# Kernel optimization log

Measured on AMD Instinct MI355X. Metric: run time of the kernel, lower is better.

The kernel has to match this reference:

```python
import jax, jax.numpy as jnp
import numpy as np

B, T, C, E, TOPK = 4, 4096, 1024, 8, 2
H = 4 * C

def setup_inputs() -> dict:
    key = jax.random.key(0)
    ks = jax.random.split(key, 8)
    s = 1.0 / np.sqrt(C)
    sh = 1.0 / np.sqrt(H)
    return {
        "x": jax.random.normal(ks[0], (B, T, C), jnp.float32),
        "noise_eps": jax.random.normal(ks[1], (B, T, E), jnp.float32),
        "route_w": jax.random.normal(ks[2], (C, E), jnp.float32) * s,
        "route_b": jnp.zeros((E,), jnp.float32),
        "noise_w": jax.random.normal(ks[3], (C, E), jnp.float32) * s,
        "noise_b": jnp.zeros((E,), jnp.float32),
        "w1": jax.random.normal(ks[4], (E, C, H), jnp.float32) * s,
        "b1": jnp.zeros((E, H), jnp.float32),
        "w2": jax.random.normal(ks[5], (E, H, C), jnp.float32) * sh,
        "b2": jnp.zeros((E, C), jnp.float32),
        "top_k": TOPK,
    }

def reference(x, noise_eps, route_w, route_b, noise_w, noise_b, w1, b1, w2, b2, top_k):
    Bq, Tq, Cq = x.shape
    nE = route_w.shape[1]
    xf = x.reshape(Bq * Tq, Cq)                      # [N, C]
    N = xf.shape[0]
    logits = xf @ route_w + route_b                   # [N, E]
    std = jax.nn.softplus(xf @ noise_w + noise_b)     # [N, E]
    noisy = logits + noise_eps.reshape(N, nE) * std   # [N, E]
    _, top_idx = jax.lax.top_k(noisy, top_k)          # [N, K]
    rows = jnp.arange(N)[:, None]
    mask = jnp.zeros((N, nE), bool).at[rows, top_idx].set(True)
    # softmax over only the selected logits (others -> prob 0)
    probs = jax.nn.softmax(jnp.where(mask, noisy, -jnp.inf), axis=-1)  # [N, E]
    out = jnp.zeros_like(xf)
    for e in range(nE):  # small fixed expert count
        h = jax.nn.relu(xf @ w1[e] + b1[e])           # [N, 4C]
        y = h @ w2[e] + b2[e]                         # [N, C]
        out = out + probs[:, e:e + 1] * y             # prob==0 for unrouted tokens
    return out.reshape(Bq, Tq, Cq)
```

## Files before the change

kernel.cpp:

```cpp
#include <hip/hip_runtime.h>
#include <hip/hip_bf16.h>
#include <stdint.h>

#define NC 1024
#define NE 8
#define NH 4096
#define NN 16384

typedef __bf16 bf16x8_t __attribute__((ext_vector_type(8)));
typedef float f32x4_t __attribute__((ext_vector_type(4)));

__device__ __forceinline__ void cvt8(const float4 a, const float4 b, __bf16* dst) {
  bf16x8_t r;
  r[0] = (__bf16)a.x; r[1] = (__bf16)a.y; r[2] = (__bf16)a.z; r[3] = (__bf16)a.w;
  r[4] = (__bf16)b.x; r[5] = (__bf16)b.y; r[6] = (__bf16)b.z; r[7] = (__bf16)b.w;
  *(bf16x8_t*)dst = r;
}

__global__ __launch_bounds__(256) void routing_kernel(
    const float* __restrict__ x, const float* __restrict__ eps,
    const float* __restrict__ rw, const float* __restrict__ rb,
    const float* __restrict__ nw, const float* __restrict__ nb,
    int* __restrict__ eidx, float2* __restrict__ pp2) {
  const int lane = threadIdx.x & 63;
  const int n = blockIdx.x * 4 + (threadIdx.x >> 6);
  if (n >= NN) return;
  double acc[16];
#pragma unroll
  for (int i = 0; i < 16; ++i) acc[i] = 0.0;
  const float* xr = x + (size_t)n * NC;
  for (int c0 = 0; c0 < NC; c0 += 64) {
    const int c = c0 + lane;
    const float xv = xr[c];
    const float4 r0 = *(const float4*)(rw + (size_t)c * NE);
    const float4 r1 = *(const float4*)(rw + (size_t)c * NE + 4);
    const float4 n0 = *(const float4*)(nw + (size_t)c * NE);
    const float4 n1 = *(const float4*)(nw + (size_t)c * NE + 4);
    acc[0] += (double)xv * r0.x;  acc[1] += (double)xv * r0.y;
    acc[2] += (double)xv * r0.z;  acc[3] += (double)xv * r0.w;
    acc[4] += (double)xv * r1.x;  acc[5] += (double)xv * r1.y;
    acc[6] += (double)xv * r1.z;  acc[7] += (double)xv * r1.w;
    acc[8] += (double)xv * n0.x;  acc[9] += (double)xv * n0.y;
    acc[10] += (double)xv * n0.z; acc[11] += (double)xv * n0.w;
    acc[12] += (double)xv * n1.x; acc[13] += (double)xv * n1.y;
    acc[14] += (double)xv * n1.z; acc[15] += (double)xv * n1.w;
  }
#pragma unroll
  for (int off = 32; off > 0; off >>= 1) {
#pragma unroll
    for (int i = 0; i < 16; ++i) acc[i] += __shfl_xor(acc[i], off, 64);
  }
  if (lane == 0) {
    double noisy[NE];
#pragma unroll
    for (int e = 0; e < NE; ++e) {
      const double lg = acc[e] + (double)rb[e];
      const double z = acc[8 + e] + (double)nb[e];
      const double sp = log1p(exp(-fabs(z))) + fmax(z, 0.0);
      noisy[e] = lg + (double)eps[(size_t)n * NE + e] * sp;
    }
    int i1 = -1, i2 = -1;
    double v1 = -1e300, v2 = -1e300;
#pragma unroll
    for (int e = 0; e < NE; ++e) {
      const double v = noisy[e];
      if (v > v1) { v2 = v1; i2 = i1; v1 = v; i1 = e; }
      else if (v > v2) { v2 = v; i2 = e; }
    }
    if (i1 < 0) i1 = 0;
    if (i2 < 0 || i2 == i1) i2 = (i1 + 1) & 7;
    const double d = exp(v2 - v1);
    const float p1 = (float)(1.0 / (1.0 + d));
    const float p2 = (float)(d / (1.0 + d));
    eidx[n] = i1 | (i2 << 8);
    pp2[n] = float2{p1, p2};
  }
}

__global__ __launch_bounds__(256) void build_lists(
    const int* __restrict__ eidx, const float2* __restrict__ pp2,
    int* __restrict__ counts, int* __restrict__ perm, float* __restrict__ pprob) {
  __shared__ int hist[NE];
  __shared__ int base[NE];
  const int t = threadIdx.x;
  if (t < NE) hist[t] = 0;
  __syncthreads();
  const int n = blockIdx.x * 256 + t;
  const int packed = eidx[n];
  const int e1 = packed & 255;
  const int e2 = (packed >> 8) & 255;
  const float2 p = pp2[n];
  const int l1 = atomicAdd(&hist[e1], 1);
  const int l2 = atomicAdd(&hist[e2], 1);
  __syncthreads();
  if (t < NE) base[t] = atomicAdd(&counts[t], hist[t]);
  __syncthreads();
  const int o1 = base[e1] + l1;
  const int o2 = base[e2] + l2;
  perm[e1 * NN + o1] = n; pprob[e1 * NN + o1] = p.x;
  perm[e2 * NN + o2] = n; pprob[e2 * NN + o2] = p.y;
}

__global__ __launch_bounds__(256) void transpose_cvt(
    const float* __restrict__ src, __bf16* __restrict__ dst, int R, int Cc) {
  __shared__ __align__(16) __bf16 tile[64][72];
  const int r0 = blockIdx.y * 64, c0 = blockIdx.x * 64;
  const int t = threadIdx.x;
  const int tr = t >> 3;
  const int tc = (t & 7) * 8;
#pragma unroll
  for (int h = 0; h < 2; ++h) {
    const int r = tr + h * 32;
    const float* sp = src + (size_t)(r0 + r) * Cc + (c0 + tc);
    const float4 a = *(const float4*)sp;
    const float4 b = *(const float4*)(sp + 4);
    cvt8(a, b, &tile[r][tc]);
  }
  __syncthreads();
#pragma unroll
  for (int h = 0; h < 2; ++h) {
    const int c = tr + h * 32;
    __bf16 tmp[8] __attribute__((aligned(16)));
#pragma unroll
    for (int j = 0; j < 8; ++j) tmp[j] = tile[tc + j][c];
    __bf16* dp = dst + (size_t)(c0 + c) * R + (r0 + tc);
    *(uint4*)dp = *(const uint4*)tmp;
  }
}

template<bool FASTB>
__global__ __launch_bounds__(256) void moe_gemm1(
    const float* __restrict__ x, const void* __restrict__ bsrc,
    const float* __restrict__ bias, __bf16* __restrict__ hbuf,
    const int* __restrict__ counts_e, const int* __restrict__ perm_e, int chunk_start) {
  int cnt = *counts_e; if (cnt > NN) cnt = NN; if (cnt < 0) cnt = 0;
  const int lr0 = blockIdx.y * 128;
  const int row0 = chunk_start + lr0;
  if (row0 >= cnt) return;
  const int t = threadIdx.x;

  __shared__ __align__(16) __bf16 As[128 * 32];
  __shared__ __align__(16) __bf16 Bs[128 * 32];

  const int ar1 = row0 + (t >> 2), ar2 = ar1 + 64;
  const int tokA = (ar1 < cnt) ? perm_e[ar1] : 0;
  const int tokB = (ar2 < cnt) ? perm_e[ar2] : 0;
  const int kg = (t & 3) * 8;
  const float* pA1 = x + (size_t)tokA * NC + kg;
  const float* pA2 = x + (size_t)tokB * NC + kg;
  const int n0 = blockIdx.x * 128;

  const __bf16* pB1 = nullptr; const __bf16* pB2 = nullptr;
  const float* pBw = nullptr;
  const int kk = t >> 3, cc = (t & 7) * 16;
  if (FASTB) {
    const __bf16* bt = (const __bf16*)bsrc;
    const int nrow = n0 + (t >> 2);
    pB1 = bt + (size_t)nrow * NC + kg;
    pB2 = bt + (size_t)(nrow + 64) * NC + kg;
  } else {
    pBw = (const float*)bsrc + (size_t)kk * NH + n0 + cc;
  }

  f32x4_t acc[4][4];
#pragma unroll
  for (int i = 0; i < 4; ++i)
#pragma unroll
    for (int j = 0; j < 4; ++j)
#pragma unroll
      for (int k = 0; k < 4; ++k) acc[i][j][k] = 0.f;

  const int lane = t & 63, wid = t >> 6;
  const int wm = (wid >> 1) * 64, wn = (wid & 1) * 64;
  const int col16 = lane & 15, quad = lane >> 4;
  const int a_off = (wm + col16) * 32 + quad * 8;
  const int b_off = (wn + col16) * 32 + quad * 8;

  for (int k0 = 0; k0 < NC; k0 += 32) {
    const float4 a1a = *(const float4*)(pA1 + k0);
    const float4 a1b = *(const float4*)(pA1 + k0 + 4);
    const float4 a2a = *(const float4*)(pA2 + k0);
    const float4 a2b = *(const float4*)(pA2 + k0 + 4);
    uint4 vb1, vb2; float4 w0, w1, w2, w3;
    if (FASTB) {
      vb1 = *(const uint4*)(pB1 + k0);
      vb2 = *(const uint4*)(pB2 + k0);
    } else {
      const float* pw = pBw + (size_t)k0 * NH;
      w0 = *(const float4*)pw; w1 = *(const float4*)(pw + 4);
      w2 = *(const float4*)(pw + 8); w3 = *(const float4*)(pw + 12);
    }
    __syncthreads();
    cvt8(a1a, a1b, As + t * 8);
    cvt8(a2a, a2b, As + 2048 + t * 8);
    if (FASTB) {
      *(uint4*)(Bs + t * 8) = vb1;
      *(uint4*)(Bs + 2048 + t * 8) = vb2;
    } else {
      cvt8(w0, w1, Bs + kk * 128 + cc);
      cvt8(w2, w3, Bs + kk * 128 + cc + 8);
    }
    __syncthreads();
    bf16x8_t af[4], bfr[4];
#pragma unroll
    for (int mi = 0; mi < 4; ++mi) af[mi] = *(const bf16x8_t*)(As + a_off + mi * 512);
    if (FASTB) {
#pragma unroll
      for (int ni = 0; ni < 4; ++ni) bfr[ni] = *(const bf16x8_t*)(Bs + b_off + ni * 512);
    } else {
#pragma unroll
      for (int ni = 0; ni < 4; ++ni) {
        const int bn = wn + ni * 16 + col16;
#pragma unroll
        for (int j = 0; j < 8; ++j) bfr[ni][j] = Bs[(quad * 8 + j) * 128 + bn];
      }
    }
#pragma unroll
    for (int mi = 0; mi < 4; ++mi)
#pragma unroll
      for (int ni = 0; ni < 4; ++ni)
        acc[mi][ni] = __builtin_amdgcn_mfma_f32_16x16x32_bf16(af[mi], bfr[ni], acc[mi][ni], 0, 0, 0);
  }

  const int colbase = n0 + wn + col16;
#pragma unroll
  for (int mi = 0; mi < 4; ++mi)
#pragma unroll
    for (int reg = 0; reg < 4; ++reg) {
      const int lr = lr0 + wm + mi * 16 + quad * 4 + reg;
      if (chunk_start + lr < cnt) {
        __bf16* hp = hbuf + (size_t)lr * NH + colbase;
#pragma unroll
        for (int ni = 0; ni < 4; ++ni) {
          const float v = acc[mi][ni][reg] + bias[colbase + ni * 16];
          hp[ni * 16] = (__bf16)fmaxf(v, 0.f);
        }
      }
    }
}

template<bool FASTB>
__global__ __launch_bounds__(256) void moe_gemm2(
    const __bf16* __restrict__ hbuf, const void* __restrict__ bsrc,
    const float* __restrict__ bias, float* __restrict__ out,
    const int* __restrict__ counts_e, const int* __restrict__ perm_e,
    const float* __restrict__ pprob_e, int chunk_start) {
  int cnt = *counts_e; if (cnt > NN) cnt = NN; if (cnt < 0) cnt = 0;
  const int lr0 = blockIdx.y * 128;
  if (chunk_start + lr0 >= cnt) return;
  const int t = threadIdx.x;

  __shared__ __align__(16) __bf16 As[128 * 32];
  __shared__ __align__(16) __bf16 Bs[128 * 32];

  const int lar1 = lr0 + (t >> 2);
  const int kg = (t & 3) * 8;
  const __bf16* pA1 = hbuf + (size_t)lar1 * NH + kg;
  const __bf16* pA2 = pA1 + (size_t)64 * NH;
  const int n0 = blockIdx.x * 128;

  const __bf16* pB1 = nullptr; const __bf16* pB2 = nullptr;
  const float* pBw = nullptr;
  const int kk = t >> 3, cc = (t & 7) * 16;
  if (FASTB) {
    const __bf16* bt = (const __bf16*)bsrc;
    const int nrow = n0 + (t >> 2);
    pB1 = bt + (size_t)nrow * NH + kg;
    pB2 = bt + (size_t)(nrow + 64) * NH + kg;
  } else {
    pBw = (const float*)bsrc + (size_t)kk * NC + n0 + cc;
  }

  f32x4_t acc[4][4];
#pragma unroll
  for (int i = 0; i < 4; ++i)
#pragma unroll
    for (int j = 0; j < 4; ++j)
#pragma unroll
      for (int k = 0; k < 4; ++k) acc[i][j][k] = 0.f;

  const int lane = t & 63, wid = t >> 6;
  const int wm = (wid >> 1) * 64, wn = (wid & 1) * 64;
  const int col16 = lane & 15, quad = lane >> 4;
  const int a_off = (wm + col16) * 32 + quad * 8;
  const int b_off = (wn + col16) * 32 + quad * 8;

  for (int k0 = 0; k0 < NH; k0 += 32) {
    const uint4 va1 = *(const uint4*)(pA1 + k0);
    const uint4 va2 = *(const uint4*)(pA2 + k0);
    uint4 vb1, vb2; float4 w0, w1, w2, w3;
    if (FASTB) {
      vb1 = *(const uint4*)(pB1 + k0);
      vb2 = *(const uint4*)(pB2 + k0);
    } else {
      const float* pw = pBw + (size_t)k0 * NC;
      w0 = *(const float4*)pw; w1 = *(const float4*)(pw + 4);
      w2 = *(const float4*)(pw + 8); w3 = *(const float4*)(pw + 12);
    }
    __syncthreads();
    *(uint4*)(As + t * 8) = va1;
    *(uint4*)(As + 2048 + t * 8) = va2;
    if (FASTB) {
      *(uint4*)(Bs + t * 8) = vb1;
      *(uint4*)(Bs + 2048 + t * 8) = vb2;
    } else {
      cvt8(w0, w1, Bs + kk * 128 + cc);
      cvt8(w2, w3, Bs + kk * 128 + cc + 8);
    }
    __syncthreads();
    bf16x8_t af[4], bfr[4];
#pragma unroll
    for (int mi = 0; mi < 4; ++mi) af[mi] = *(const bf16x8_t*)(As + a_off + mi * 512);
    if (FASTB) {
#pragma unroll
      for (int ni = 0; ni < 4; ++ni) bfr[ni] = *(const bf16x8_t*)(Bs + b_off + ni * 512);
    } else {
#pragma unroll
      for (int ni = 0; ni < 4; ++ni) {
        const int bn = wn + ni * 16 + col16;
#pragma unroll
        for (int j = 0; j < 8; ++j) bfr[ni][j] = Bs[(quad * 8 + j) * 128 + bn];
      }
    }
#pragma unroll
    for (int mi = 0; mi < 4; ++mi)
#pragma unroll
      for (int ni = 0; ni < 4; ++ni)
        acc[mi][ni] = __builtin_amdgcn_mfma_f32_16x16x32_bf16(af[mi], bfr[ni], acc[mi][ni], 0, 0, 0);
  }

  const int colbase = n0 + wn + col16;
#pragma unroll
  for (int mi = 0; mi < 4; ++mi)
#pragma unroll
    for (int reg = 0; reg < 4; ++reg) {
      const int lr = lr0 + wm + mi * 16 + quad * 4 + reg;
      const int r = chunk_start + lr;
      if (r < cnt) {
        const int tok = perm_e[r];
        const float p = pprob_e[r];
        float* op = out + (size_t)tok * NC + colbase;
#pragma unroll
        for (int ni = 0; ni < 4; ++ni) {
          op[ni * 16] += (acc[mi][ni][reg] + bias[colbase + ni * 16]) * p;
        }
      }
    }
}

extern "C" void kernel_launch(void* const* d_in, const int* in_sizes, int n_in,
                              void* d_out, int out_size, void* d_ws, size_t ws_size,
                              hipStream_t stream) {
  (void)in_sizes; (void)n_in;
  const float* x   = (const float*)d_in[0];
  const float* eps = (const float*)d_in[1];
  const float* rw  = (const float*)d_in[2];
  const float* rb  = (const float*)d_in[3];
  const float* nw  = (const float*)d_in[4];
  const float* nb  = (const float*)d_in[5];
  const float* w1  = (const float*)d_in[6];
  const float* b1  = (const float*)d_in[7];
  const float* w2  = (const float*)d_in[8];
  const float* b2  = (const float*)d_in[9];
  float* out = (float*)d_out;

  char* wsb = (char*)d_ws;
  int* counts = (int*)wsb;
  int* perm = (int*)(wsb + 256);
  float* pprob = (float*)(wsb + 256 + (size_t)NE * NN * 4);
  int* eidx = (int*)(wsb + 256 + (size_t)NE * NN * 8);
  float2* pp2 = (float2*)(wsb + 256 + (size_t)NE * NN * 8 + (size_t)NN * 4);
  size_t off = 256 + (size_t)NE * NN * 8 + (size_t)NN * 12;

  const size_t wtile = (size_t)NC * NH * 2;
  const bool fast = ws_size >= off + 2 * wtile + (size_t)128 * NH * 2 + (1u << 20);
  __bf16* w1t = nullptr; __bf16* w2t = nullptr;
  if (fast) {
    w1t = (__bf16*)(wsb + off); off += wtile;
    w2t = (__bf16*)(wsb + off); off += wtile;
  }
  __bf16* hbuf = (__bf16*)(wsb + off);
  const size_t remain = (ws_size > off) ? (ws_size - off) : 0;
  long rows_cap = (long)(remain / ((size_t)NH * 2));
  rows_cap = (rows_cap / 128) * 128;
  if (rows_cap > NN) rows_cap = NN;
  if (rows_cap < 128) rows_cap = 128;

  hipMemsetAsync(counts, 0, 256, stream);
  hipMemsetAsync(d_out, 0, (size_t)out_size * 4, stream);

  routing_kernel<<<NN / 4, 256, 0, stream>>>(x, eps, rw, rb, nw, nb, eidx, pp2);
  build_lists<<<NN / 256, 256, 0, stream>>>(eidx, pp2, counts, perm, pprob);

  const int nchunks = (int)((NN + rows_cap - 1) / rows_cap);
  for (int e = 0; e < NE; ++e) {
    const float* w1e = w1 + (size_t)e * NC * NH;
    const float* w2e = w2 + (size_t)e * NH * NC;
    if (fast) {
      transpose_cvt<<<dim3(NH / 64, NC / 64), 256, 0, stream>>>(w1e, w1t, NC, NH);
      transpose_cvt<<<dim3(NC / 64, NH / 64), 256, 0, stream>>>(w2e, w2t, NH, NC);
    }
    for (int ch = 0; ch < nchunks; ++ch) {
      const int cs = ch * (int)rows_cap;
      if (fast) {
        moe_gemm1<true><<<dim3(NH / 128, (unsigned)(rows_cap / 128)), 256, 0, stream>>>(
            x, w1t, b1 + (size_t)e * NH, hbuf, counts + e, perm + (size_t)e * NN, cs);
        moe_gemm2<true><<<dim3(NC / 128, (unsigned)(rows_cap / 128)), 256, 0, stream>>>(
            hbuf, w2t, b2 + (size_t)e * NC, out, counts + e, perm + (size_t)e * NN,
            pprob + (size_t)e * NN, cs);
      } else {
        moe_gemm1<false><<<dim3(NH / 128, (unsigned)(rows_cap / 128)), 256, 0, stream>>>(
            x, w1e, b1 + (size_t)e * NH, hbuf, counts + e, perm + (size_t)e * NN, cs);
        moe_gemm2<false><<<dim3(NC / 128, (unsigned)(rows_cap / 128)), 256, 0, stream>>>(
            hbuf, w2e, b2 + (size_t)e * NC, out, counts + e, perm + (size_t)e * NN,
            pprob + (size_t)e * NN, cs);
      }
    }
  }
}
```

Measured before the change: 1.892 ms.

## Split-K the second expert GEMM across four wave groups with shared-memory reduction

The down-projection GEMM now launches 1024-thread blocks in which four 256-thread groups each process one quarter of the K=4096 dimension, then sum their partial accumulators through shared memory before the first group writes the output. The aim is more parallelism and memory-level concurrency for gemm2, whose grid (8 column tiles by the row tiles) is small. The cost is 64KB of LDS per block, extra reduction syncs, and 1024-thread blocks that force tighter register limits (possible spills with 64 accumulator floats per thread).

Result: no change. 1.868 ms (-1.3%).

```diff
diff --git a/kernel.cpp b/kernel.cpp
--- a/kernel.cpp
+++ b/kernel.cpp
@@ -240,7 +240,7 @@
 }
 
 template<bool FASTB>
-__global__ __launch_bounds__(256) void moe_gemm2(
+__global__ __launch_bounds__(1024) void moe_gemm2(
     const __bf16* __restrict__ hbuf, const void* __restrict__ bsrc,
     const float* __restrict__ bias, float* __restrict__ out,
     const int* __restrict__ counts_e, const int* __restrict__ perm_e,
@@ -249,26 +249,30 @@
   const int lr0 = blockIdx.y * 128;
   if (chunk_start + lr0 >= cnt) return;
   const int t = threadIdx.x;
-
-  __shared__ __align__(16) __bf16 As[128 * 32];
-  __shared__ __align__(16) __bf16 Bs[128 * 32];
-
-  const int lar1 = lr0 + (t >> 2);
-  const int kg = (t & 3) * 8;
-  const __bf16* pA1 = hbuf + (size_t)lar1 * NH + kg;
+  const int ksub = t >> 8;
+  const int tt = t & 255;
+
+  __shared__ __align__(16) __bf16 smem[32768];
+  __bf16* As = smem + ksub * 4096;
+  __bf16* Bs = smem + 16384 + ksub * 4096;
+
+  const int lar1 = lr0 + (tt >> 2);
+  const int kg = (tt & 3) * 8;
+  const int kbase = ksub * (NH / 4);
+  const __bf16* pA1 = hbuf + (size_t)lar1 * NH + kbase + kg;
   const __bf16* pA2 = pA1 + (size_t)64 * NH;
   const int n0 = blockIdx.x * 128;
 
   const __bf16* pB1 = nullptr; const __bf16* pB2 = nullptr;
   const float* pBw = nullptr;
-  const int kk = t >> 3, cc = (t & 7) * 16;
+  const int kk = tt >> 3, cc = (tt & 7) * 16;
   if (FASTB) {
     const __bf16* bt = (const __bf16*)bsrc;
-    const int nrow = n0 + (t >> 2);
-    pB1 = bt + (size_t)nrow * NH + kg;
-    pB2 = bt + (size_t)(nrow + 64) * NH + kg;
+    const int nrow = n0 + (tt >> 2);
+    pB1 = bt + (size_t)nrow * NH + kbase + kg;
+    pB2 = bt + (size_t)(nrow + 64) * NH + kbase + kg;
   } else {
-    pBw = (const float*)bsrc + (size_t)kk * NC + n0 + cc;
+    pBw = (const float*)bsrc + (size_t)(kbase + kk) * NC + n0 + cc;
   }
 
   f32x4_t acc[4][4];
@@ -279,13 +283,13 @@
 #pragma unroll
       for (int k = 0; k < 4; ++k) acc[i][j][k] = 0.f;
 
-  const int lane = t & 63, wid = t >> 6;
+  const int lane = tt & 63, wid = tt >> 6;
   const int wm = (wid >> 1) * 64, wn = (wid & 1) * 64;
   const int col16 = lane & 15, quad = lane >> 4;
   const int a_off = (wm + col16) * 32 + quad * 8;
   const int b_off = (wn + col16) * 32 + quad * 8;
 
-  for (int k0 = 0; k0 < NH; k0 += 32) {
+  for (int k0 = 0; k0 < NH / 4; k0 += 32) {
     const uint4 va1 = *(const uint4*)(pA1 + k0);
     const uint4 va2 = *(const uint4*)(pA2 + k0);
     uint4 vb1, vb2; float4 w0, w1, w2, w3;
@@ -298,11 +302,11 @@
       w2 = *(const float4*)(pw + 8); w3 = *(const float4*)(pw + 12);
     }
     __syncthreads();
-    *(uint4*)(As + t * 8) = va1;
-    *(uint4*)(As + 2048 + t * 8) = va2;
-    if (FASTB) {
-      *(uint4*)(Bs + t * 8) = vb1;
-      *(uint4*)(Bs + 2048 + t * 8) = vb2;
+    *(uint4*)(As + tt * 8) = va1;
+    *(uint4*)(As + 2048 + tt * 8) = va2;
+    if (FASTB) {
+      *(uint4*)(Bs + tt * 8) = vb1;
+      *(uint4*)(Bs + 2048 + tt * 8) = vb2;
     } else {
       cvt8(w0, w1, Bs + kk * 128 + cc);
       cvt8(w2, w3, Bs + kk * 128 + cc + 8);
@@ -328,6 +332,28 @@
       for (int ni = 0; ni < 4; ++ni)
         acc[mi][ni] = __builtin_amdgcn_mfma_f32_16x16x32_bf16(af[mi], bfr[ni], acc[mi][ni], 0, 0, 0);
   }
+
+  __syncthreads();
+  f32x4_t* red = (f32x4_t*)smem;
+  for (int r = 1; r < 4; ++r) {
+    if (ksub == r) {
+#pragma unroll
+      for (int mi = 0; mi < 4; ++mi)
+#pragma unroll
+        for (int ni = 0; ni < 4; ++ni)
+          red[(mi * 4 + ni) * 256 + tt] = acc[mi][ni];
+    }
+    __syncthreads();
+    if (ksub == 0) {
+#pragma unroll
+      for (int mi = 0; mi < 4; ++mi)
+#pragma unroll
+        for (int ni = 0; ni < 4; ++ni)
+          acc[mi][ni] += red[(mi * 4 + ni) * 256 + tt];
+    }
+    __syncthreads();
+  }
+  if (ksub != 0) return;
 
   const int colbase = n0 + wn + col16;
 #pragma unroll
@@ -405,13 +431,13 @@
       if (fast) {
         moe_gemm1<true><<<dim3(NH / 128, (unsigned)(rows_cap / 128)), 256, 0, stream>>>(
             x, w1t, b1 + (size_t)e * NH, hbuf, counts + e, perm + (size_t)e * NN, cs);
-        moe_gemm2<true><<<dim3(NC / 128, (unsigned)(rows_cap / 128)), 256, 0, stream>>>(
+        moe_gemm2<true><<<dim3(NC / 128, (unsigned)(rows_cap / 128)), 1024, 0, stream>>>(
             hbuf, w2t, b2 + (size_t)e * NC, out, counts + e, perm + (size_t)e * NN,
             pprob + (size_t)e * NN, cs);
       } else {
         moe_gemm1<false><<<dim3(NH / 128, (unsigned)(rows_cap / 128)), 256, 0, stream>>>(
             x, w1e, b1 + (size_t)e * NH, hbuf, counts + e, perm + (size_t)e * NN, cs);
-        moe_gemm2<false><<<dim3(NC / 128, (unsigned)(rows_cap / 128)), 256, 0, stream>>>(
+        moe_gemm2<false><<<dim3(NC / 128, (unsigned)(rows_cap / 128)), 1024, 0, stream>>>(
             hbuf, w2e, b2 + (size_t)e * NC, out, counts + e, perm + (size_t)e * NN,
             pprob + (size_t)e * NN, cs);
       }
```

## Double-buffer LDS tiles with register prefetch and XOR swizzle in MoE GEMMs

Applied to the files above, without the earlier changes.

In the FASTB path of both expert GEMM kernels, the shared-memory A/B tiles are now double-buffered and the next k-slice is prefetched into registers while MFMAs run, so each iteration needs one barrier instead of two. The LDS layout also gets an XOR swizzle on the 8-element column groups to cut bank conflicts on fragment reads. The cost is twice the shared memory per block, which may lower occupancy, plus more registers held live for the prefetch.

Result: faster. 1.717 ms (-9.2%).

```diff
diff --git a/kernel.cpp b/kernel.cpp
--- a/kernel.cpp
+++ b/kernel.cpp
@@ -128,6 +128,7 @@
   }
 }
 
+
 template<bool FASTB>
 __global__ __launch_bounds__(256) void moe_gemm1(
     const float* __restrict__ x, const void* __restrict__ bsrc,
@@ -139,8 +140,8 @@
   if (row0 >= cnt) return;
   const int t = threadIdx.x;
 
-  __shared__ __align__(16) __bf16 As[128 * 32];
-  __shared__ __align__(16) __bf16 Bs[128 * 32];
+  __shared__ __align__(16) __bf16 As[2 * 128 * 32];
+  __shared__ __align__(16) __bf16 Bs[2 * 128 * 32];
 
   const int ar1 = row0 + (t >> 2), ar2 = ar1 + 64;
   const int tokA = (ar1 < cnt) ? perm_e[ar1] : 0;
@@ -173,53 +174,81 @@
   const int lane = t & 63, wid = t >> 6;
   const int wm = (wid >> 1) * 64, wn = (wid & 1) * 64;
   const int col16 = lane & 15, quad = lane >> 4;
-  const int a_off = (wm + col16) * 32 + quad * 8;
-  const int b_off = (wn + col16) * 32 + quad * 8;
-
-  for (int k0 = 0; k0 < NC; k0 += 32) {
-    const float4 a1a = *(const float4*)(pA1 + k0);
-    const float4 a1b = *(const float4*)(pA1 + k0 + 4);
-    const float4 a2a = *(const float4*)(pA2 + k0);
-    const float4 a2b = *(const float4*)(pA2 + k0 + 4);
-    uint4 vb1, vb2; float4 w0, w1, w2, w3;
-    if (FASTB) {
-      vb1 = *(const uint4*)(pB1 + k0);
-      vb2 = *(const uint4*)(pB2 + k0);
-    } else {
+
+  if (FASTB) {
+    const int woff = (t >> 2) * 32 + (((t & 3) ^ ((t >> 3) & 3)) * 8);
+    const int sel = (col16 >> 1) & 3;
+    const int a_off = (wm + col16) * 32 + ((quad ^ sel) * 8);
+    const int b_off = (wn + col16) * 32 + ((quad ^ sel) * 8);
+
+    float4 a1a = *(const float4*)(pA1);
+    float4 a1b = *(const float4*)(pA1 + 4);
+    float4 a2a = *(const float4*)(pA2);
+    float4 a2b = *(const float4*)(pA2 + 4);
+    uint4 vb1 = *(const uint4*)(pB1);
+    uint4 vb2 = *(const uint4*)(pB2);
+    int cur = 0;
+    for (int k0 = 0; k0 < NC; k0 += 32) {
+      __bf16* Asc = As + cur * 4096;
+      __bf16* Bsc = Bs + cur * 4096;
+      cvt8(a1a, a1b, Asc + woff);
+      cvt8(a2a, a2b, Asc + 2048 + woff);
+      *(uint4*)(Bsc + woff) = vb1;
+      *(uint4*)(Bsc + 2048 + woff) = vb2;
+      if (k0 + 32 < NC) {
+        a1a = *(const float4*)(pA1 + k0 + 32);
+        a1b = *(const float4*)(pA1 + k0 + 36);
+        a2a = *(const float4*)(pA2 + k0 + 32);
+        a2b = *(const float4*)(pA2 + k0 + 36);
+        vb1 = *(const uint4*)(pB1 + k0 + 32);
+        vb2 = *(const uint4*)(pB2 + k0 + 32);
+      }
+      __syncthreads();
+      bf16x8_t af[4], bfr[4];
+#pragma unroll
+      for (int mi = 0; mi < 4; ++mi) af[mi] = *(const bf16x8_t*)(Asc + a_off + mi * 512);
+#pragma unroll
+      for (int ni = 0; ni < 4; ++ni) bfr[ni] = *(const bf16x8_t*)(Bsc + b_off + ni * 512);
+#pragma unroll
+      for (int mi = 0; mi < 4; ++mi)
+#pragma unroll
+        for (int ni = 0; ni < 4; ++ni)
+          acc[mi][ni] = __builtin_amdgcn_mfma_f32_16x16x32_bf16(af[mi], bfr[ni], acc[mi][ni], 0, 0, 0);
+      cur ^= 1;
+    }
+  } else {
+    const int a_off = (wm + col16) * 32 + quad * 8;
+    for (int k0 = 0; k0 < NC; k0 += 32) {
+      const float4 a1a = *(const float4*)(pA1 + k0);
+      const float4 a1b = *(const float4*)(pA1 + k0 + 4);
+      const float4 a2a = *(const float4*)(pA2 + k0);
+      const float4 a2b = *(const float4*)(pA2 + k0 + 4);
       const float* pw = pBw + (size_t)k0 * NH;
-      w0 = *(const float4*)pw; w1 = *(const float4*)(pw + 4);
-      w2 = *(const float4*)(pw + 8); w3 = *(const float4*)(pw + 12);
-    }
-    __syncthreads();
-    cvt8(a1a, a1b, As + t * 8);
-    cvt8(a2a, a2b, As + 2048 + t * 8);
-    if (FASTB) {
-      *(uint4*)(Bs + t * 8) = vb1;
-      *(uint4*)(Bs + 2048 + t * 8) = vb2;
-    } else {
+      const float4 w0 = *(const float4*)pw;
+      const float4 w1 = *(const float4*)(pw + 4);
+      const float4 w2 = *(const float4*)(pw + 8);
+      const float4 w3 = *(const float4*)(pw + 12);
+      __syncthreads();
+      cvt8(a1a, a1b, As + t * 8);
+      cvt8(a2a, a2b, As + 2048 + t * 8);
       cvt8(w0, w1, Bs + kk * 128 + cc);
       cvt8(w2, w3, Bs + kk * 128 + cc + 8);
-    }
-    __syncthreads();
-    bf16x8_t af[4], bfr[4];
-#pragma unroll
-    for (int mi = 0; mi < 4; ++mi) af[mi] = *(const bf16x8_t*)(As + a_off + mi * 512);
-    if (FASTB) {
-#pragma unroll
-      for (int ni = 0; ni < 4; ++ni) bfr[ni] = *(const bf16x8_t*)(Bs + b_off + ni * 512);
-    } else {
+      __syncthreads();
+      bf16x8_t af[4], bfr[4];
+#pragma unroll
+      for (int mi = 0; mi < 4; ++mi) af[mi] = *(const bf16x8_t*)(As + a_off + mi * 512);
 #pragma unroll
       for (int ni = 0; ni < 4; ++ni) {
         const int bn = wn + ni * 16 + col16;
 #pragma unroll
         for (int j = 0; j < 8; ++j) bfr[ni][j] = Bs[(quad * 8 + j) * 128 + bn];
       }
-    }
-#pragma unroll
-    for (int mi = 0; mi < 4; ++mi)
-#pragma unroll
-      for (int ni = 0; ni < 4; ++ni)
-        acc[mi][ni] = __builtin_amdgcn_mfma_f32_16x16x32_bf16(af[mi], bfr[ni], acc[mi][ni], 0, 0, 0);
+#pragma unroll
+      for (int mi = 0; mi < 4; ++mi)
+#pragma unroll
+        for (int ni = 0; ni < 4; ++ni)
+          acc[mi][ni] = __builtin_amdgcn_mfma_f32_16x16x32_bf16(af[mi], bfr[ni], acc[mi][ni], 0, 0, 0);
+    }
   }
 
   const int colbase = n0 + wn + col16;
@@ -250,8 +279,8 @@
   if (chunk_start + lr0 >= cnt) return;
   const int t = threadIdx.x;
 
-  __shared__ __align__(16) __bf16 As[128 * 32];
-  __shared__ __align__(16) __bf16 Bs[128 * 32];
+  __shared__ __align__(16) __bf16 As[2 * 128 * 32];
+  __shared__ __align__(16) __bf16 Bs[2 * 128 * 32];
 
   const int lar1 = lr0 + (t >> 2);
   const int kg = (t & 3) * 8;
@@ -282,51 +311,75 @@
   const int lane = t & 63, wid = t >> 6;
   const int wm = (wid >> 1) * 64, wn = (wid & 1) * 64;
   const int col16 = lane & 15, quad = lane >> 4;
-  const int a_off = (wm + col16) * 32 + quad * 8;
-  const int b_off = (wn + col16) * 32 + quad * 8;
-
-  for (int k0 = 0; k0 < NH; k0 += 32) {
-    const uint4 va1 = *(const uint4*)(pA1 + k0);
-    const uint4 va2 = *(const uint4*)(pA2 + k0);
-    uint4 vb1, vb2; float4 w0, w1, w2, w3;
-    if (FASTB) {
-      vb1 = *(const uint4*)(pB1 + k0);
-      vb2 = *(const uint4*)(pB2 + k0);
-    } else {
+
+  if (FASTB) {
+    const int woff = (t >> 2) * 32 + (((t & 3) ^ ((t >> 3) & 3)) * 8);
+    const int sel = (col16 >> 1) & 3;
+    const int a_off = (wm + col16) * 32 + ((quad ^ sel) * 8);
+    const int b_off = (wn + col16) * 32 + ((quad ^ sel) * 8);
+
+    uint4 va1 = *(const uint4*)(pA1);
+    uint4 va2 = *(const uint4*)(pA2);
+    uint4 vb1 = *(const uint4*)(pB1);
+    uint4 vb2 = *(const uint4*)(pB2);
+    int cur = 0;
+    for (int k0 = 0; k0 < NH; k0 += 32) {
+      __bf16* Asc = As + cur * 4096;
+      __bf16* Bsc = Bs + cur * 4096;
+      *(uint4*)(Asc + woff) = va1;
+      *(uint4*)(Asc + 2048 + woff) = va2;
+      *(uint4*)(Bsc + woff) = vb1;
+      *(uint4*)(Bsc + 2048 + woff) = vb2;
+      if (k0 + 32 < NH) {
+        va1 = *(const uint4*)(pA1 + k0 + 32);
+        va2 = *(const uint4*)(pA2 + k0 + 32);
+        vb1 = *(const uint4*)(pB1 + k0 + 32);
+        vb2 = *(const uint4*)(pB2 + k0 + 32);
+      }
+      __syncthreads();
+      bf16x8_t af[4], bfr[4];
+#pragma unroll
+      for (int mi = 0; mi < 4; ++mi) af[mi] = *(const bf16x8_t*)(Asc + a_off + mi * 512);
+#pragma unroll
+      for (int ni = 0; ni < 4; ++ni) bfr[ni] = *(const bf16x8_t*)(Bsc + b_off + ni * 512);
+#pragma unroll
+      for (int mi = 0; mi < 4; ++mi)
+#pragma unroll
+        for (int ni = 0; ni < 4; ++ni)
+          acc[mi][ni] = __builtin_amdgcn_mfma_f32_16x16x32_bf16(af[mi], bfr[ni], acc[mi][ni], 0, 0, 0);
+      cur ^= 1;
+    }
+  } else {
+    const int a_off = (wm + col16) * 32 + quad * 8;
+    for (int k0 = 0; k0 < NH; k0 += 32) {
+      const uint4 va1 = *(const uint4*)(pA1 + k0);
+      const uint4 va2 = *(const uint4*)(pA2 + k0);
       const float* pw = pBw + (size_t)k0 * NC;
-      w0 = *(const float4*)pw; w1 = *(const float4*)(pw + 4);
-      w2 = *(const float4*)(pw + 8); w3 = *(const float4*)(pw + 12);
-    }
-    __syncthreads();
-    *(uint4*)(As + t * 8) = va1;
-    *(uint4*)(As + 2048 + t * 8) = va2;
-    if (FASTB) {
-      *(uint4*)(Bs + t * 8) = vb1;
-      *(uint4*)(Bs + 2048 + t * 8) = vb2;
-    } else {
+      const float4 w0 = *(const float4*)pw;
+      const float4 w1 = *(const float4*)(pw + 4);
+      const float4 w2 = *(const float4*)(pw + 8);
+      const float4 w3 = *(const float4*)(pw + 12);
+      __syncthreads();
+      *(uint4*)(As + t * 8) = va1;
+      *(uint4*)(As + 2048 + t * 8) = va2;
       cvt8(w0, w1, Bs + kk * 128 + cc);
       cvt8(w2, w3, Bs + kk * 128 + cc + 8);
-    }
-    __syncthreads();
-    bf16x8_t af[4], bfr[4];
-#pragma unroll
-    for (int mi = 0; mi < 4; ++mi) af[mi] = *(const bf16x8_t*)(As + a_off + mi * 512);
-    if (FASTB) {
-#pragma unroll
-      for (int ni = 0; ni < 4; ++ni) bfr[ni] = *(const bf16x8_t*)(Bs + b_off + ni * 512);
-    } else {
+      __syncthreads();
+      bf16x8_t af[4], bfr[4];
+#pragma unroll
+      for (int mi = 0; mi < 4; ++mi) af[mi] = *(const bf16x8_t*)(As + a_off + mi * 512);
 #pragma unroll
       for (int ni = 0; ni < 4; ++ni) {
         const int bn = wn + ni * 16 + col16;
 #pragma unroll
         for (int j = 0; j < 8; ++j) bfr[ni][j] = Bs[(quad * 8 + j) * 128 + bn];
       }
-    }
-#pragma unroll
-    for (int mi = 0; mi < 4; ++mi)
-#pragma unroll
-      for (int ni = 0; ni < 4; ++ni)
-        acc[mi][ni] = __builtin_amdgcn_mfma_f32_16x16x32_bf16(af[mi], bfr[ni], acc[mi][ni], 0, 0, 0);
+#pragma unroll
+      for (int mi = 0; mi < 4; ++mi)
+#pragma unroll
+        for (int ni = 0; ni < 4; ++ni)
+          acc[mi][ni] = __builtin_amdgcn_mfma_f32_16x16x32_bf16(af[mi], bfr[ni], acc[mi][ni], 0, 0, 0);
+    }
   }
 
   const int colbase = n0 + wn + col16;
```
